# Kernel tuning notes

Measured on AMD Instinct MI355X. Metric: run time of the kernel, lower is better.

Reference implementation:

```python
import jax, jax.numpy as jnp
import numpy as np

N = 4096     # nagents
OBS = 256    # obs_size
HID = 256    # hid_size
G = 64       # gat_hid_size
H1 = 4       # gat_num_heads (so H1*G == HID)
H2 = 1       # gat_num_heads_out
A = 64       # actions
QMAX = 255.0  # 2**quant_bits - 1, quant_min = 0
NEG_SLOPE = 0.2


def _lstm_cell(x, h, c, Wih, Whh, bih, bhh):
    gates = x @ Wih.T + bih + h @ Whh.T + bhh
    i, f, g, o = jnp.split(gates, 4, axis=-1)
    c2 = jax.nn.sigmoid(f) * c + jax.nn.sigmoid(i) * jnp.tanh(g)
    h2 = jax.nn.sigmoid(o) * jnp.tanh(c2)
    return h2, c2


def _gat(x, adj, W, a_i, a_j, b, average, self_loop_type):
    # x: [n, in], adj: [n, n], W: [in, H*g], a_i/a_j: [H, g], b: [H*g] or [g_out]
    n = x.shape[0]
    H, g = a_i.shape
    eye = jnp.eye(n, dtype=adj.dtype)
    if self_loop_type == 1:      # force self-loops
        adj = adj * (1.0 - eye) + eye
    elif self_loop_type == 2:    # remove self-loops
        adj = adj * (1.0 - eye)
    h = (x @ W).reshape(n, H, g)                      # [n, H, g]
    ci = jnp.einsum('nhg,hg->hn', h, a_i)             # [H, n]
    cj = jnp.einsum('nhg,hg->hn', h, a_j)             # [H, n]
    e = jax.nn.leaky_relu(ci[:, :, None] + cj[:, None, :], NEG_SLOPE)  # [H, n, n]
    att = jax.nn.softmax(jnp.where(adj[None] > 0, e, -9e15), axis=-1) * adj[None]
    out = jnp.einsum('hij,jhg->ihg', att, h)          # [n, H, g]
    out = out.mean(axis=1) if average else out.reshape(n, H * g)
    return out + b


def _fake_quant(t, bmask):
    # dynamic-range fake quantization over masked entries (min/max detached)
    big = jnp.asarray(1e30, t.dtype)
    mn = jax.lax.stop_gradient(jnp.min(jnp.where(bmask, t, big)))
    mx = jax.lax.stop_gradient(jnp.max(jnp.where(bmask, t, -big)))
    eq = mn == mx
    mn = jnp.where(eq, mn - 0.01, mn)
    mx = jnp.where(eq, mx + 0.01, mx)
    scale = (mx - mn) / QMAX
    zp = jnp.round(-mn / scale)  # quant_min = 0
    deq = (jnp.clip(jnp.round(t / scale + zp), 0.0, QMAX) - zp) * scale
    return jnp.where(bmask, deq, t)


def _qloss(t, bmask):
    return jnp.sum(jnp.where(bmask, jnp.log2(2.0 * QMAX * jnp.abs(t) + 1.0), 0.0))


def _forward(obs, h0, c0, Wobs, bobs, Wih, Whh, bih, bhh,
             W1, ai1, aj1, b1, W2, ai2, aj2, b2, Wv, bv, Wa, ba):
    n = N
    mask = jnp.ones((n, 1), obs.dtype)        # all agents alive
    enc = obs.reshape(n, -1) @ Wobs + bobs    # obs encoder, squeeze batch=1
    h, c = _lstm_cell(enc, h0, c0, Wih, Whh, bih, bhh)
    comm = h
    bmask = jnp.broadcast_to(mask > 0, comm.shape)
    comm = _fake_quant(comm, bmask)
    loss = _qloss(comm, bmask)
    comm = comm * mask
    adj = jnp.ones((n, n), obs.dtype) * mask * mask.T   # complete graph
    comm = _gat(comm, adj, W1, ai1, aj1, b1, average=False, self_loop_type=1)
    comm = jax.nn.elu(comm)
    bmask2 = jnp.broadcast_to(mask > 0, comm.shape)
    comm = _fake_quant(comm, bmask2)
    loss = loss + _qloss(comm, bmask2)
    comm = _gat(comm, adj, W2, ai2, aj2, b2, average=True, self_loop_type=1)
    comm = comm * mask
    value = jnp.concatenate([h, comm], axis=-1) @ Wv + bv              # [n, 1]
    feat = jnp.concatenate([h.reshape(1, n, -1), comm.reshape(1, n, -1)], axis=-1)
    logp = jax.nn.log_softmax(feat @ Wa + ba, axis=-1)                 # [1, n, A]
    return logp, value, h, c, loss


def setup_inputs() -> dict:
    key = jax.random.key(0)
    ks = jax.random.split(key, 21)
    def rn(k, shape, sc=0.05):
        return jax.random.normal(k, shape, dtype=jnp.float32) * sc
    return {
        'obs': rn(ks[0], (1, N, OBS), 1.0),
        'h0': rn(ks[1], (N, HID), 1.0),
        'c0': rn(ks[2], (N, HID), 1.0),
        'Wobs': rn(ks[3], (OBS, HID)),
        'bobs': rn(ks[4], (HID,)),
        'Wih': rn(ks[5], (4 * HID, HID)),
        'Whh': rn(ks[6], (4 * HID, HID)),
        'bih': rn(ks[7], (4 * HID,)),
        'bhh': rn(ks[8], (4 * HID,)),
        'W1': rn(ks[9], (HID, H1 * G)),
        'ai1': rn(ks[10], (H1, G)),
        'aj1': rn(ks[11], (H1, G)),
        'b1': rn(ks[12], (H1 * G,)),
        'W2': rn(ks[13], (H1 * G, H2 * HID)),
        'ai2': rn(ks[14], (H2, HID)),
        'aj2': rn(ks[15], (H2, HID)),
        'b2': rn(ks[16], (HID,)),
        'Wv': rn(ks[17], (2 * HID, 1)),
        'bv': rn(ks[18], (1,)),
        'Wa': rn(ks[19], (2 * HID, A)),
        'ba': rn(ks[20], (A,)),
    }


def reference(obs, h0, c0, Wobs, bobs, Wih, Whh, bih, bhh,
              W1, ai1, aj1, b1, W2, ai2, aj2, b2, Wv, bv, Wa, ba):
    return _forward(obs, h0, c0, Wobs, bobs, Wih, Whh, bih, bhh,
                    W1, ai1, aj1, b1, W2, ai2, aj2, b2, Wv, bv, Wa, ba)
```

## Files before the change

### kernel.cpp

```cpp
#include <hip/hip_runtime.h>
#include <math.h>

typedef __attribute__((ext_vector_type(8))) short short8;
typedef __attribute__((ext_vector_type(4))) float floatx4;

__device__ __forceinline__ ushort f2b(float f) {
  unsigned u = __float_as_uint(f);
  unsigned r = u + 0x7FFFu + ((u >> 16) & 1u);
  return (ushort)(r >> 16);
}
__device__ __forceinline__ unsigned encf(float f) {
  unsigned u = __float_as_uint(f);
  return (u & 0x80000000u) ? ~u : (u | 0x80000000u);
}
__device__ __forceinline__ float b2f(ushort b) {
  return __uint_as_float(((unsigned)b) << 16);
}

__global__ __launch_bounds__(256) void prep_kernel(
    const float* __restrict__ Wih, ushort* __restrict__ Wihp,
    const float* __restrict__ Whh, ushort* __restrict__ Whhp,
    const float* __restrict__ Wobs, ushort* __restrict__ WobsT,
    const float* __restrict__ W1, ushort* __restrict__ W1T,
    const float* __restrict__ W2, ushort* __restrict__ W2T,
    const float* __restrict__ Wa, const float* __restrict__ Wv,
    const float* __restrict__ ba, const float* __restrict__ bv,
    const float* __restrict__ bih, const float* __restrict__ bhh,
    ushort* __restrict__ WaTe, float* __restrict__ bias_ext, float* __restrict__ bias12,
    const float* __restrict__ ai1, const float* __restrict__ aj1,
    const float* __restrict__ ai2, const float* __restrict__ aj2,
    ushort* __restrict__ wab1, ushort* __restrict__ wab2)
{
  __shared__ float tile[32][33];
  const int bid = blockIdx.x;
  const int tid = threadIdx.x;
  if (bid < 512) {
    const int i = bid * 256 + tid;
    const int half = i >> 16;
    const int ii = i & 65535;
    const int pr = ii >> 6, k4 = ii & 63;
    const int orow = ((pr >> 4) & 3) * 256 + (pr >> 6) * 16 + (pr & 15);
    const float* s = half ? Whh : Wih;
    ushort* d = half ? Whhp : Wihp;
    const float4 v = *(const float4*)(s + (size_t)orow * 256 + k4 * 4);
    ushort4 o; o.x = f2b(v.x); o.y = f2b(v.y); o.z = f2b(v.z); o.w = f2b(v.w);
    *(ushort4*)(d + (size_t)pr * 256 + k4 * 4) = o;
  } else if (bid < 704) {
    const int t = bid - 512;
    const int mat = t >> 6, sub = t & 63;
    const float* in = mat == 0 ? Wobs : (mat == 1 ? W1 : W2);
    ushort* outp = mat == 0 ? WobsT : (mat == 1 ? W1T : W2T);
    const int c0 = (sub & 7) * 32, r0 = (sub >> 3) * 32;
    const int tx = tid & 31, ty = tid >> 5;
    #pragma unroll
    for (int p = 0; p < 32; p += 8)
      tile[ty + p][tx] = in[(size_t)(r0 + ty + p) * 256 + c0 + tx];
    __syncthreads();
    #pragma unroll
    for (int p = 0; p < 32; p += 8)
      outp[(size_t)(c0 + ty + p) * 256 + r0 + tx] = f2b(tile[tx][ty + p]);
  } else if (bid < 965) {
    const int idx = (bid - 704) * 256 + tid;
    if (idx < 65536) {
      const int n = idx >> 9, k = idx & 511;
      const float v = n < 64 ? Wa[(size_t)k * 64 + n] : (n == 64 ? Wv[k] : 0.0f);
      WaTe[idx] = f2b(v);
    } else if (idx < 65536 + 128) {
      const int n = idx - 65536;
      bias_ext[n] = n < 64 ? ba[n] : (n == 64 ? bv[0] : 0.0f);
    } else if (idx < 65536 + 128 + 1024) {
      const int pc = idx - 65536 - 128;
      const int orow = ((pc >> 4) & 3) * 256 + (pc >> 6) * 16 + (pc & 15);
      bias12[pc] = bih[orow] + bhh[orow];
    }
  } else if (bid < 981) {
    const int c = bid - 965;
    const int k = tid;
    float val = 0.0f;
    if (c < 8) {
      const int h = c & 3;
      const float* av = (c < 4) ? ai1 : aj1;
      for (int g = 0; g < 64; ++g)
        val += W1[(size_t)k * 256 + h * 64 + g] * av[h * 64 + g];
    }
    wab1[c * 256 + k] = f2b(val);
  } else {
    const int c = bid - 981;
    const int k = tid;
    float val = 0.0f;
    if (c < 2) {
      const float* av = (c == 0) ? ai2 : aj2;
      for (int g = 0; g < 256; ++g)
        val += W2[(size_t)k * 256 + g] * av[g];
    }
    wab2[c * 256 + k] = f2b(val);
  }
}

__global__ __launch_bounds__(256) void enc_gemm(
    const float* __restrict__ obs, const ushort* __restrict__ WobsT,
    const float* __restrict__ bobs, ushort* __restrict__ enc_bf)
{
  constexpr int LDT = 40;
  __shared__ __align__(16) ushort As[64 * LDT];
  __shared__ __align__(16) ushort Bs[64 * LDT];
  const int tid = threadIdx.x;
  const int wave = tid >> 6, lane = tid & 63;
  const int wr = wave >> 1, wc = wave & 1;
  const int m0 = blockIdx.y * 64, n0 = blockIdx.x * 64;
  floatx4 acc[2][2] = {};
  const int r = tid >> 2, kq = tid & 3;
  const int lm = lane & 15, lq = lane >> 4;
  for (int k0 = 0; k0 < 256; k0 += 32) {
    {
      const float* s = &obs[(size_t)(m0 + r) * 256 + k0 + kq * 8];
      const float4 a = *(const float4*)s;
      const float4 b = *(const float4*)(s + 4);
      ushort4 o1, o2;
      o1.x = f2b(a.x); o1.y = f2b(a.y); o1.z = f2b(a.z); o1.w = f2b(a.w);
      o2.x = f2b(b.x); o2.y = f2b(b.y); o2.z = f2b(b.z); o2.w = f2b(b.w);
      *(ushort4*)&As[r * LDT + kq * 8] = o1;
      *(ushort4*)&As[r * LDT + kq * 8 + 4] = o2;
      *(float4*)&Bs[r * LDT + kq * 8] =
          *(const float4*)&WobsT[(size_t)(n0 + r) * 256 + k0 + kq * 8];
    }
    __syncthreads();
    short8 af[2], bfr[2];
    #pragma unroll
    for (int i = 0; i < 2; ++i)
      af[i] = *(const short8*)&As[(wr * 32 + i * 16 + lm) * LDT + lq * 8];
    #pragma unroll
    for (int j = 0; j < 2; ++j)
      bfr[j] = *(const short8*)&Bs[(wc * 32 + j * 16 + lm) * LDT + lq * 8];
    #pragma unroll
    for (int i = 0; i < 2; ++i)
      #pragma unroll
      for (int j = 0; j < 2; ++j)
        acc[i][j] = __builtin_amdgcn_mfma_f32_16x16x32_bf16(af[i], bfr[j], acc[i][j], 0, 0, 0);
    __syncthreads();
  }
  #pragma unroll
  for (int i = 0; i < 2; ++i)
    #pragma unroll
    for (int j = 0; j < 2; ++j) {
      const int col = n0 + wc * 32 + j * 16 + lm;
      const float badd = bobs[col];
      #pragma unroll
      for (int t = 0; t < 4; ++t) {
        const int row = m0 + wr * 32 + i * 16 + lq * 4 + t;
        enc_bf[(size_t)row * 256 + col] = f2b(acc[i][j][t] + badd);
      }
    }
}

__global__ __launch_bounds__(256) void gates_lstm_kernel(
    const ushort* __restrict__ enc_bf, const ushort* __restrict__ Wihp,
    const float* __restrict__ h0, const ushort* __restrict__ Whhp,
    const float* __restrict__ bias12p, const float* __restrict__ c0,
    float* __restrict__ h_out, float* __restrict__ c_out, ushort* __restrict__ h_bf,
    float* __restrict__ pmn, float* __restrict__ pmx)
{
  constexpr int LDT = 40;
  __shared__ __align__(16) ushort As[128 * LDT];
  __shared__ __align__(16) ushort Bs[128 * LDT];
  __shared__ float smn[4], smx[4];
  const int tid = threadIdx.x;
  const int wave = tid >> 6, lane = tid & 63;
  const int wr = wave >> 1, wc = wave & 1;
  const int m0 = blockIdx.y * 128, n0 = blockIdx.x * 128;
  floatx4 acc[4][4] = {};
  const int r = tid >> 2, kq = tid & 3;
  const int lm = lane & 15, lq = lane >> 4;
  for (int k0 = 0; k0 < 512; k0 += 32) {
    const ushort* B = (k0 < 256) ? Wihp : Whhp;
    const int kk = (k0 < 256) ? k0 : k0 - 256;
    if (k0 < 256) {
      #pragma unroll
      for (int p = 0; p < 2; ++p) {
        const int rr = r + p * 64;
        *(float4*)&As[rr * LDT + kq * 8] =
            *(const float4*)&enc_bf[(size_t)(m0 + rr) * 256 + kk + kq * 8];
      }
    } else {
      #pragma unroll
      for (int p = 0; p < 2; ++p) {
        const int rr = r + p * 64;
        const float* s = &h0[(size_t)(m0 + rr) * 256 + kk + kq * 8];
        const float4 a = *(const float4*)s;
        const float4 b = *(const float4*)(s + 4);
        ushort4 o1, o2;
        o1.x = f2b(a.x); o1.y = f2b(a.y); o1.z = f2b(a.z); o1.w = f2b(a.w);
        o2.x = f2b(b.x); o2.y = f2b(b.y); o2.z = f2b(b.z); o2.w = f2b(b.w);
        *(ushort4*)&As[rr * LDT + kq * 8] = o1;
        *(ushort4*)&As[rr * LDT + kq * 8 + 4] = o2;
      }
    }
    #pragma unroll
    for (int p = 0; p < 2; ++p) {
      const int rr = r + p * 64;
      *(float4*)&Bs[rr * LDT + kq * 8] =
          *(const float4*)&B[(size_t)(n0 + rr) * 256 + kk + kq * 8];
    }
    __syncthreads();
    short8 af[4], bfr[4];
    #pragma unroll
    for (int i = 0; i < 4; ++i)
      af[i] = *(const short8*)&As[(wr * 64 + i * 16 + lm) * LDT + lq * 8];
    #pragma unroll
    for (int j = 0; j < 4; ++j)
      bfr[j] = *(const short8*)&Bs[(wc * 64 + j * 16 + lm) * LDT + lq * 8];
    #pragma unroll
    for (int i = 0; i < 4; ++i)
      #pragma unroll
      for (int j = 0; j < 4; ++j)
        acc[i][j] = __builtin_amdgcn_mfma_f32_16x16x32_bf16(af[i], bfr[j], acc[i][j], 0, 0, 0);
    __syncthreads();
  }
  const int d = (blockIdx.x * 2 + wc) * 16 + lm;
  float b4[4];
  #pragma unroll
  for (int j = 0; j < 4; ++j) b4[j] = bias12p[n0 + wc * 64 + j * 16 + lm];
  float mnl = 3.0e38f, mxl = -3.0e38f;
  #pragma unroll
  for (int i = 0; i < 4; ++i) {
    #pragma unroll
    for (int t = 0; t < 4; ++t) {
      const int row = m0 + wr * 64 + i * 16 + lq * 4 + t;
      const size_t off = (size_t)row * 256 + d;
      const float gi = acc[i][0][t] + b4[0];
      const float gf = acc[i][1][t] + b4[1];
      const float gg = acc[i][2][t] + b4[2];
      const float go = acc[i][3][t] + b4[3];
      const float cc = c0[off];
      const float si = 1.0f / (1.0f + expf(-gi));
      const float sf = 1.0f / (1.0f + expf(-gf));
      const float so = 1.0f / (1.0f + expf(-go));
      const float c2 = sf * cc + si * tanhf(gg);
      const float h2 = so * tanhf(c2);
      h_out[off] = h2;
      c_out[off] = c2;
      h_bf[off] = f2b(h2);
      mnl = fminf(mnl, h2); mxl = fmaxf(mxl, h2);
    }
  }
  #pragma unroll
  for (int o = 32; o > 0; o >>= 1) {
    mnl = fminf(mnl, __shfl_xor(mnl, o));
    mxl = fmaxf(mxl, __shfl_xor(mxl, o));
  }
  if (lane == 0) { smn[wave] = mnl; smx[wave] = mxl; }
  __syncthreads();
  if (tid == 0) {
    const int bid = blockIdx.y * 8 + blockIdx.x;
    pmn[bid] = fminf(fminf(smn[0], smn[1]), fminf(smn[2], smn[3]));
    pmx[bid] = fmaxf(fmaxf(smx[0], smx[1]), fmaxf(smx[2], smx[3]));
  }
}

__global__ __launch_bounds__(256) void quant_kernel(
    const float4* __restrict__ x, ushort* __restrict__ q, int n4,
    const float* __restrict__ pmn, const float* __restrict__ pmx, int np,
    float* __restrict__ part)
{
  __shared__ float smn[4], smx[4], sl[4], bmn, bmx;
  float mn = 3.0e38f, mx = -3.0e38f;
  for (int i = threadIdx.x; i < np; i += 256) {
    mn = fminf(mn, pmn[i]); mx = fmaxf(mx, pmx[i]);
  }
  #pragma unroll
  for (int o = 32; o > 0; o >>= 1) {
    mn = fminf(mn, __shfl_xor(mn, o));
    mx = fmaxf(mx, __shfl_xor(mx, o));
  }
  if ((threadIdx.x & 63) == 0) { smn[threadIdx.x >> 6] = mn; smx[threadIdx.x >> 6] = mx; }
  __syncthreads();
  if (threadIdx.x == 0) {
    bmn = fminf(fminf(smn[0], smn[1]), fminf(smn[2], smn[3]));
    bmx = fmaxf(fmaxf(smx[0], smx[1]), fmaxf(smx[2], smx[3]));
  }
  __syncthreads();
  mn = bmn; mx = bmx;
  if (mn == mx) { mn -= 0.01f; mx += 0.01f; }
  const float scale = (mx - mn) / 255.0f;
  const float zp = rintf(-mn / scale);
  float lsum = 0.0f;
  for (int idx = blockIdx.x * 256 + threadIdx.x; idx < n4; idx += gridDim.x * 256) {
    const float4 t = x[idx];
    float d0, d1, d2, d3;
    { float qq = fminf(fmaxf(rintf(t.x / scale + zp), 0.0f), 255.0f);
      d0 = (qq - zp) * scale; lsum += log2f(510.0f * fabsf(d0) + 1.0f); }
    { float qq = fminf(fmaxf(rintf(t.y / scale + zp), 0.0f), 255.0f);
      d1 = (qq - zp) * scale; lsum += log2f(510.0f * fabsf(d1) + 1.0f); }
    { float qq = fminf(fmaxf(rintf(t.z / scale + zp), 0.0f), 255.0f);
      d2 = (qq - zp) * scale; lsum += log2f(510.0f * fabsf(d2) + 1.0f); }
    { float qq = fminf(fmaxf(rintf(t.w / scale + zp), 0.0f), 255.0f);
      d3 = (qq - zp) * scale; lsum += log2f(510.0f * fabsf(d3) + 1.0f); }
    ushort4 o; o.x = f2b(d0); o.y = f2b(d1); o.z = f2b(d2); o.w = f2b(d3);
    *(ushort4*)(q + (size_t)idx * 4) = o;
  }
  #pragma unroll
  for (int o = 32; o > 0; o >>= 1) lsum += __shfl_xor(lsum, o);
  if ((threadIdx.x & 63) == 0) sl[threadIdx.x >> 6] = lsum;
  __syncthreads();
  if (threadIdx.x == 0) part[blockIdx.x] = sl[0] + sl[1] + sl[2] + sl[3];
}

template<int HN>
__global__ __launch_bounds__(256) void gat_feat_kernel(
    const ushort* __restrict__ Aq, const ushort* __restrict__ WT,
    const ushort* __restrict__ wab,
    float* __restrict__ hout, float* __restrict__ ci, float* __restrict__ cj)
{
  constexpr int LDT = 40;
  __shared__ __align__(16) ushort As[64 * LDT];
  __shared__ __align__(16) ushort Bs[64 * LDT];
  const int bid = blockIdx.x;
  const int tid = threadIdx.x;
  const int wave = tid >> 6, lane = tid & 63;
  const int lm = lane & 15, lq = lane >> 4;
  const int r = tid >> 2, kq = tid & 3;
  if (bid < 256) {
    const int bx = bid & 3, by = bid >> 2;
    const int m0 = by * 64, n0 = bx * 64;
    const int wr = wave >> 1, wc = wave & 1;
    floatx4 acc[2][2] = {};
    for (int k0 = 0; k0 < 256; k0 += 32) {
      *(float4*)&As[r * LDT + kq * 8] =
          *(const float4*)&Aq[(size_t)(m0 + r) * 256 + k0 + kq * 8];
      *(float4*)&Bs[r * LDT + kq * 8] =
          *(const float4*)&WT[(size_t)(n0 + r) * 256 + k0 + kq * 8];
      __syncthreads();
      short8 af[2], bfr[2];
      #pragma unroll
      for (int i = 0; i < 2; ++i)
        af[i] = *(const short8*)&As[(wr * 32 + i * 16 + lm) * LDT + lq * 8];
      #pragma unroll
      for (int j = 0; j < 2; ++j)
        bfr[j] = *(const short8*)&Bs[(wc * 32 + j * 16 + lm) * LDT + lq * 8];
      #pragma unroll
      for (int i = 0; i < 2; ++i)
        #pragma unroll
        for (int j = 0; j < 2; ++j)
          acc[i][j] = __builtin_amdgcn_mfma_f32_16x16x32_bf16(af[i], bfr[j], acc[i][j], 0, 0, 0);
      __syncthreads();
    }
    #pragma unroll
    for (int i = 0; i < 2; ++i)
      #pragma unroll
      for (int j = 0; j < 2; ++j) {
        const int col = n0 + wc * 32 + j * 16 + lm;
        #pragma unroll
        for (int t = 0; t < 4; ++t) {
          const int row = m0 + wr * 32 + i * 16 + lq * 4 + t;
          hout[(size_t)row * 256 + col] = acc[i][j][t];
        }
      }
  } else {
    const int m0 = (bid - 256) * 64;
    floatx4 acc = {0.f, 0.f, 0.f, 0.f};
    for (int k0 = 0; k0 < 256; k0 += 32) {
      *(float4*)&As[r * LDT + kq * 8] =
          *(const float4*)&Aq[(size_t)(m0 + r) * 256 + k0 + kq * 8];
      if (r < 16)
        *(float4*)&Bs[r * LDT + kq * 8] =
            *(const float4*)&wab[(size_t)r * 256 + k0 + kq * 8];
      __syncthreads();
      const short8 af = *(const short8*)&As[(wave * 16 + lm) * LDT + lq * 8];
      const short8 bf = *(const short8*)&Bs[lm * LDT + lq * 8];
      acc = __builtin_amdgcn_mfma_f32_16x16x32_bf16(af, bf, acc, 0, 0, 0);
      __syncthreads();
    }
    #pragma unroll
    for (int t = 0; t < 4; ++t) {
      const int row = m0 + wave * 16 + lq * 4 + t;
      if (lm < HN) ci[lm * 4096 + row] = acc[t];
      else if (lm < 2 * HN) cj[(lm - HN) * 4096 + row] = acc[t];
    }
  }
}

__global__ __launch_bounds__(1024) void rank_sort_kernel(
    const float* __restrict__ c, unsigned* __restrict__ skey,
    float* __restrict__ sc, int* __restrict__ pm)
{
  __shared__ unsigned lk[4096];
  __shared__ int scnt[16][64];
  const int head = blockIdx.x >> 6;
  const int seg = blockIdx.x & 63;
  const float* ch = c + head * 4096;
  for (int idx = threadIdx.x; idx < 4096; idx += 1024)
    lk[idx] = (encf(ch[idx]) & 0xFFFFF000u) | (unsigned)idx;
  __syncthreads();
  const int jl = threadIdx.x & 63;
  const int kg = threadIdx.x >> 6;
  const unsigned my = lk[seg * 64 + jl];
  int cnt = 0;
  const int k0 = kg * 256;
  #pragma unroll 8
  for (int k = k0; k < k0 + 256; ++k)
    cnt += lk[k] < my ? 1 : 0;
  scnt[kg][jl] = cnt;
  __syncthreads();
  if (threadIdx.x < 64) {
    int rank = 0;
    #pragma unroll
    for (int g = 0; g < 16; ++g) rank += scnt[g][threadIdx.x];
    const unsigned kk = lk[seg * 64 + threadIdx.x];
    const int jj = (int)(kk & 0xFFFu);
    skey[head * 4096 + rank] = kk;
    sc[head * 4096 + rank] = ch[jj];
    pm[head * 4096 + rank] = jj;
  }
}

__global__ __launch_bounds__(128) void local_scan1(
    const float* __restrict__ h1, const float* __restrict__ sc, const int* __restrict__ pm,
    float* __restrict__ PUl, float* __restrict__ PVl,
    float* __restrict__ dUl, float* __restrict__ dVl,
    float* __restrict__ cku, float* __restrict__ ckv,
    float* __restrict__ ckus, float* __restrict__ ckvs)
{
  const int head = blockIdx.x >> 6;
  const int chunk = blockIdx.x & 63;
  const int wave = threadIdx.x >> 6;
  const int lane = threadIdx.x & 63;
  const float cmax = sc[head * 4096 + 4095];
  const int base = head * 4096 + chunk * 64;
  const float cv = sc[base + lane];
  const float u = expf(cv - cmax);
  const float v = expf(0.2f * (cv - cmax));
  const int myj = pm[base + lane];
  const float* hrow = h1 + head * 64 + lane;
  if (wave == 0) {
    float iu = u, iv = v;
    #pragma unroll
    for (int o = 1; o < 64; o <<= 1) {
      const float tu = __shfl_up(iu, o), tv = __shfl_up(iv, o);
      if (lane >= o) { iu += tu; iv += tv; }
    }
    const float totU = __shfl(iu, 63), totV = __shfl(iv, 63);
    dVl[base + lane] = iv - v;
    dUl[base + lane] = totU - (iu - u);
    if (lane == 0) { ckus[head * 64 + chunk] = totU; ckvs[head * 64 + chunk] = totV; }
    float accV = 0.f;
    #pragma unroll 16
    for (int k = 0; k < 64; ++k) {
      const float vk = __shfl(v, k);
      const int j = __shfl(myj, k);
      PVl[(size_t)(base + k) * 64 + lane] = accV;
      accV += vk * hrow[(size_t)j * 256];
    }
    ckv[(head * 64 + chunk) * 64 + lane] = accV;
  } else {
    float accU = 0.f;
    #pragma unroll 16
    for (int k = 63; k >= 0; --k) {
      const float uk = __shfl(u, k);
      const int j = __shfl(myj, k);
      accU += uk * hrow[(size_t)j * 256];
      PUl[(size_t)(base + k) * 64 + lane] = accU;
    }
    cku[(head * 64 + chunk) * 64 + lane] = accU;
  }
}

__global__ __launch_bounds__(256) void local_scan2(
    const float* __restrict__ h2, const float* __restrict__ sc, const int* __restrict__ pm,
    float* __restrict__ PUl, float* __restrict__ PVl,
    float* __restrict__ dUl, float* __restrict__ dVl,
    float* __restrict__ cku, float* __restrict__ ckv,
    float* __restrict__ ckus, float* __restrict__ ckvs)
{
  __shared__ float su[64], sv[64];
  __shared__ int sj[64];
  const int chunk = blockIdx.y;
  const int colgrp = blockIdx.x;
  const int tid = threadIdx.x;
  const int wave = tid >> 6, lane = tid & 63;
  const float cmax = sc[4095];
  const int base = chunk * 64;
  if (tid < 64) {
    const float cv = sc[base + tid];
    const float u = expf(cv - cmax);
    const float v = expf(0.2f * (cv - cmax));
    su[tid] = u; sv[tid] = v; sj[tid] = pm[base + tid];
    if (colgrp == 0) {
      float iu = u, iv = v;
      #pragma unroll
      for (int o = 1; o < 64; o <<= 1) {
        const float tu = __shfl_up(iu, o), tv = __shfl_up(iv, o);
        if (lane >= o) { iu += tu; iv += tv; }
      }
      const float totU = __shfl(iu, 63), totV = __shfl(iv, 63);
      dVl[base + lane] = iv - v;
      dUl[base + lane] = totU - (iu - u);
      if (lane == 0) { ckus[chunk] = totU; ckvs[chunk] = totV; }
    }
  }
  __syncthreads();
  const int col = colgrp * 128 + (wave & 1) * 64 + lane;
  if (wave < 2) {
    float accV = 0.f;
    #pragma unroll 16
    for (int k = 0; k < 64; ++k) {
      PVl[(size_t)(base + k) * 256 + col] = accV;
      accV += sv[k] * h2[(size_t)sj[k] * 256 + col];
    }
    ckv[chunk * 256 + col] = accV;
  } else {
    float accU = 0.f;
    #pragma unroll 16
    for (int k = 63; k >= 0; --k) {
      accU += su[k] * h2[(size_t)sj[k] * 256 + col];
      PUl[(size_t)(base + k) * 256 + col] = accU;
    }
    cku[chunk * 256 + col] = accU;
  }
}

__global__ __launch_bounds__(64) void prefix1_kernel(
    const float* __restrict__ cku, const float* __restrict__ ckv,
    const float* __restrict__ ckus, const float* __restrict__ ckvs,
    float* __restrict__ sufU, float* __restrict__ prefV,
    float* __restrict__ sufUs, float* __restrict__ prefVs)
{
  const int head = blockIdx.x, lane = threadIdx.x;
  float acc = 0.f;
  for (int c = 0; c < 64; ++c) {
    prefV[(head * 65 + c) * 64 + lane] = acc;
    acc += ckv[(head * 64 + c) * 64 + lane];
  }
  prefV[(head * 65 + 64) * 64 + lane] = acc;
  acc = 0.f;
  sufU[(head * 65 + 64) * 64 + lane] = 0.f;
  for (int c = 63; c >= 0; --c) {
    acc += cku[(head * 64 + c) * 64 + lane];
    sufU[(head * 65 + c) * 64 + lane] = acc;
  }
  {
    const float vs = ckvs[head * 64 + lane];
    const float us = ckus[head * 64 + lane];
    float iv = vs, iu = us;
    #pragma unroll
    for (int o = 1; o < 64; o <<= 1) {
      const float tv = __shfl_up(iv, o), tu = __shfl_up(iu, o);
      if (lane >= o) { iv += tv; iu += tu; }
    }
    prefVs[head * 65 + lane] = iv - vs;
    const float totU = __shfl(iu, 63);
    sufUs[head * 65 + lane] = totU - iu + us;
    if (lane == 63) {
      prefVs[head * 65 + 64] = iv;
      sufUs[head * 65 + 64] = 0.f;
    }
  }
}

__global__ __launch_bounds__(256) void prefix2_kernel(
    const float* __restrict__ cku, const float* __restrict__ ckv,
    const float* __restrict__ ckus, const float* __restrict__ ckvs,
    float* __restrict__ sufU, float* __restrict__ prefV,
    float* __restrict__ sufUs, float* __restrict__ prefVs)
{
  const int col = threadIdx.x;
  const int lane = col & 63;
  float acc = 0.f;
  for (int c = 0; c < 64; ++c) {
    prefV[c * 256 + col] = acc;
    acc += ckv[c * 256 + col];
  }
  prefV[64 * 256 + col] = acc;
  acc = 0.f;
  sufU[64 * 256 + col] = 0.f;
  for (int c = 63; c >= 0; --c) {
    acc += cku[c * 256 + col];
    sufU[c * 256 + col] = acc;
  }
  if (col < 64) {
    const float vs = ckvs[lane];
    const float us = ckus[lane];
    float iv = vs, iu = us;
    #pragma unroll
    for (int o = 1; o < 64; o <<= 1) {
      const float tv = __shfl_up(iv, o), tu = __shfl_up(iu, o);
      if (lane >= o) { iv += tv; iu += tu; }
    }
    prefVs[lane] = iv - vs;
    const float totU = __shfl(iu, 63);
    sufUs[lane] = totU - iu + us;
    if (lane == 63) { prefVs[64] = iv; sufUs[64] = 0.f; }
  }
}

__global__ __launch_bounds__(256) void combine1_kernel(
    const float* __restrict__ ci, const unsigned* __restrict__ skey,
    const float* __restrict__ sc,
    const float* __restrict__ sufU, const float* __restrict__ prefV,
    const float* __restrict__ sufUs, const float* __restrict__ prefVs,
    const float* __restrict__ PUl, const float* __restrict__ PVl,
    const float* __restrict__ dUl, const float* __restrict__ dVl,
    const float* __restrict__ b1, float* __restrict__ out,
    float* __restrict__ pmn, float* __restrict__ pmx)
{
  const int i = blockIdx.x;
  const int head = threadIdx.x >> 6;
  const int lane = threadIdx.x & 63;
  const unsigned* skh = skey + head * 4096;
  const float civ = ci[head * 4096 + i];
  const float cmax = sc[head * 4096 + 4095];
  const float sarg = civ + cmax;
  const float m = sarg > 0.f ? sarg : 0.2f * sarg;
  const float Af = expf(sarg - m);
  const float Bf = expf(0.2f * sarg - m);
  const unsigned tkey = (encf(-civ) & 0xFFFFF000u) | 0xFFFu;
  int lo = 0, hi = 4096;
  while (lo < hi) {
    const int mid = (lo + hi) >> 1;
    if (skh[mid] > tkey) hi = mid; else lo = mid + 1;
  }
  const int s = lo;
  float accP, accN, dP, dN;
  if (s == 4096) {
    accP = 0.f; dP = 0.f;
    accN = prefV[(head * 65 + 64) * 64 + lane];
    dN = prefVs[head * 65 + 64];
  } else {
    const int cs = s >> 6;
    accP = sufU[(head * 65 + cs + 1) * 64 + lane] + PUl[(size_t)(head * 4096 + s) * 64 + lane];
    accN = prefV[(head * 65 + cs) * 64 + lane] + PVl[(size_t)(head * 4096 + s) * 64 + lane];
    dP = sufUs[head * 65 + cs + 1] + dUl[head * 4096 + s];
    dN = prefVs[head * 65 + cs] + dVl[head * 4096 + s];
  }
  const float num = Af * accP + Bf * accN;
  const float den = Af * dP + Bf * dN;
  const float o = num / den + b1[head * 64 + lane];
  const float oe = o > 0.f ? o : expm1f(o);
  out[(size_t)i * 256 + head * 64 + lane] = oe;
  float mn = oe, mx = oe;
  #pragma unroll
  for (int of = 32; of > 0; of >>= 1) {
    mn = fminf(mn, __shfl_xor(mn, of));
    mx = fmaxf(mx, __shfl_xor(mx, of));
  }
  __shared__ float smn[4], smx[4];
  if (lane == 0) { smn[head] = mn; smx[head] = mx; }
  __syncthreads();
  if (threadIdx.x == 0) {
    pmn[i] = fminf(fminf(smn[0], smn[1]), fminf(smn[2], smn[3]));
    pmx[i] = fmaxf(fmaxf(smx[0], smx[1]), fmaxf(smx[2], smx[3]));
  }
}

__global__ __launch_bounds__(256) void combine2_kernel(
    const float* __restrict__ ci, const unsigned* __restrict__ skey,
    const float* __restrict__ sc,
    const float* __restrict__ sufU, const float* __restrict__ prefV,
    const float* __restrict__ sufUs, const float* __restrict__ prefVs,
    const float* __restrict__ PUl, const float* __restrict__ PVl,
    const float* __restrict__ dUl, const float* __restrict__ dVl,
    const float* __restrict__ b2, ushort* __restrict__ outb)
{
  const int i = blockIdx.x;
  const int col = threadIdx.x;
  const float civ = ci[i];
  const float cmax = sc[4095];
  const float sarg = civ + cmax;
  const float m = sarg > 0.f ? sarg : 0.2f * sarg;
  const float Af = expf(sarg - m);
  const float Bf = expf(0.2f * sarg - m);
  const unsigned tkey = (encf(-civ) & 0xFFFFF000u) | 0xFFFu;
  int lo = 0, hi = 4096;
  while (lo < hi) {
    const int mid = (lo + hi) >> 1;
    if (skey[mid] > tkey) hi = mid; else lo = mid + 1;
  }
  const int s = lo;
  float accP, accN, dP, dN;
  if (s == 4096) {
    accP = 0.f; dP = 0.f;
    accN = prefV[64 * 256 + col];
    dN = prefVs[64];
  } else {
    const int cs = s >> 6;
    accP = sufU[(cs + 1) * 256 + col] + PUl[(size_t)s * 256 + col];
    accN = prefV[cs * 256 + col] + PVl[(size_t)s * 256 + col];
    dP = sufUs[cs + 1] + dUl[s];
    dN = prefVs[cs] + dVl[s];
  }
  const float num = Af * accP + Bf * accN;
  const float den = Af * dP + Bf * dN;
  outb[(size_t)i * 256 + col] = f2b(num / den + b2[col]);
}

__global__ __launch_bounds__(256) void heads_kernel(
    const ushort* __restrict__ h_bf, const ushort* __restrict__ comm2_bf,
    const ushort* __restrict__ WaTe, const float* __restrict__ bias_ext,
    float* __restrict__ out_logp, float* __restrict__ out_value,
    const float* __restrict__ p1, const float* __restrict__ p2,
    float* __restrict__ out_loss)
{
  constexpr int LDT = 40;
  __shared__ __align__(16) ushort As[64 * LDT];
  __shared__ __align__(16) ushort Bs[128 * LDT];
  __shared__ float lbuf[64][68];
  const int tid = threadIdx.x;
  const int wave = tid >> 6, lane = tid & 63;
  const int wr = wave >> 1, wc = wave & 1;
  const int m0 = blockIdx.x * 64;
  const int lm = lane & 15, lq = lane >> 4;
  floatx4 acc[2][4] = {};
  const int r = tid >> 2, kq = tid & 3;
  for (int k0 = 0; k0 < 512; k0 += 32) {
    const ushort* Asrc = (k0 < 256) ? h_bf : comm2_bf;
    const int kk = (k0 < 256) ? k0 : k0 - 256;
    *(float4*)&As[r * LDT + kq * 8] =
        *(const float4*)&Asrc[(size_t)(m0 + r) * 256 + kk + kq * 8];
    #pragma unroll
    for (int p = 0; p < 2; ++p) {
      const int rr = r + p * 64;
      *(float4*)&Bs[rr * LDT + kq * 8] =
          *(const float4*)&WaTe[(size_t)rr * 512 + k0 + kq * 8];
    }
    __syncthreads();
    short8 af[2], bfr[4];
    #pragma unroll
    for (int i = 0; i < 2; ++i)
      af[i] = *(const short8*)&As[(wr * 32 + i * 16 + lm) * LDT + lq * 8];
    #pragma unroll
    for (int j = 0; j < 4; ++j)
      bfr[j] = *(const short8*)&Bs[(wc * 64 + j * 16 + lm) * LDT + lq * 8];
    #pragma unroll
    for (int i = 0; i < 2; ++i)
      #pragma unroll
      for (int j = 0; j < 4; ++j)
        acc[i][j] = __builtin_amdgcn_mfma_f32_16x16x32_bf16(af[i], bfr[j], acc[i][j], 0, 0, 0);
    __syncthreads();
  }
  #pragma unroll
  for (int i = 0; i < 2; ++i)
    #pragma unroll
    for (int j = 0; j < 4; ++j) {
      const int col = wc * 64 + j * 16 + lm;
      if (col < 65) {
        const float badd = bias_ext[col];
        #pragma unroll
        for (int t = 0; t < 4; ++t)
          lbuf[wr * 32 + i * 16 + lq * 4 + t][col] = acc[i][j][t] + badd;
      }
    }
  __syncthreads();
  for (int rr2 = 0; rr2 < 16; ++rr2) {
    const int row = wave * 16 + rr2;
    const float x = lbuf[row][lane];
    float mx = x;
    #pragma unroll
    for (int o = 32; o > 0; o >>= 1) mx = fmaxf(mx, __shfl_xor(mx, o));
    float e = expf(x - mx);
    #pragma unroll
    for (int o = 32; o > 0; o >>= 1) e += __shfl_xor(e, o);
    out_logp[(size_t)(m0 + row) * 64 + lane] = x - mx - logf(e);
    if (lane == 0) out_value[m0 + row] = lbuf[row][64];
  }
  if (blockIdx.x == 0 && wave == 0) {
    float s = 0.f;
    #pragma unroll
    for (int k = 0; k < 4; ++k) s += p1[lane + k * 64] + p2[lane + k * 64];
    #pragma unroll
    for (int o = 32; o > 0; o >>= 1) s += __shfl_xor(s, o);
    if (lane == 0) out_loss[0] = s;
  }
}

extern "C" void kernel_launch(void* const* d_in, const int* in_sizes, int n_in,
                              void* d_out, int out_size, void* d_ws, size_t ws_size,
                              hipStream_t stream) {
  const float* obs  = (const float*)d_in[0];
  const float* h0   = (const float*)d_in[1];
  const float* c0   = (const float*)d_in[2];
  const float* Wobs = (const float*)d_in[3];
  const float* bobs = (const float*)d_in[4];
  const float* Wih  = (const float*)d_in[5];
  const float* Whh  = (const float*)d_in[6];
  const float* bih  = (const float*)d_in[7];
  const float* bhh  = (const float*)d_in[8];
  const float* W1   = (const float*)d_in[9];
  const float* ai1  = (const float*)d_in[10];
  const float* aj1  = (const float*)d_in[11];
  const float* b1   = (const float*)d_in[12];
  const float* W2   = (const float*)d_in[13];
  const float* ai2  = (const float*)d_in[14];
  const float* aj2  = (const float*)d_in[15];
  const float* b2   = (const float*)d_in[16];
  const float* Wv   = (const float*)d_in[17];
  const float* bv   = (const float*)d_in[18];
  const float* Wa   = (const float*)d_in[19];
  const float* ba   = (const float*)d_in[20];

  float* out       = (float*)d_out;
  float* out_logp  = out;
  float* out_value = out + 262144;
  float* out_h     = out + 266240;
  float* out_c     = out + 1314816;
  float* out_loss  = out + 2363392;

  char* ws = (char*)d_ws;
  float* part1  = (float*)(ws + 256);
  float* part2  = (float*)(ws + 1280);
  float* pmn    = (float*)(ws + 2304);
  float* pmx    = (float*)(ws + 18688);
  const size_t MB = 1048576;
  const size_t base = 35072;
  ushort* Wihp    = (ushort*)(ws + base);
  ushort* Whhp    = (ushort*)(ws + base + 524288);
  ushort* WobsT   = (ushort*)(ws + base + 1 * MB);
  ushort* W1T     = (ushort*)(ws + base + 1 * MB + 131072);
  ushort* W2T     = (ushort*)(ws + base + 1 * MB + 262144);
  ushort* WaTe    = (ushort*)(ws + base + 1 * MB + 393216);
  float*  bias_ext= (float*) (ws + base + 1 * MB + 524288);
  float*  bias12  = (float*) (ws + base + 1 * MB + 525312);
  ushort* wab1    = (ushort*)(ws + base + 1 * MB + 532480);
  ushort* wab2    = (ushort*)(ws + base + 1 * MB + 540672);
  ushort* enc_bf  = (ushort*)(ws + base + 2 * MB);
  ushort* h_bf    = (ushort*)(ws + base + 4 * MB);
  ushort* comm_q1 = (ushort*)(ws + base + 6 * MB);
  ushort* comm_q2 = (ushort*)(ws + base + 8 * MB);
  ushort* comm2_bf= (ushort*)(ws + base + 10 * MB);
  float*  h1      = (float*) (ws + base + 12 * MB);
  float*  comm1e  = (float*) (ws + base + 16 * MB);
  float*  h2b     = (float*) (ws + base + 20 * MB);
  size_t so = base + 24 * MB;
  auto alloc = [&](size_t bytes) { size_t r = so; so += (bytes + 255) & ~255ull; return (char*)ws + r; };
  float* ci1    = (float*)alloc(4 * 4096 * 4);
  float* cj1    = (float*)alloc(4 * 4096 * 4);
  unsigned* skey1 = (unsigned*)alloc(4 * 4096 * 4);
  float* sc1    = (float*)alloc(4 * 4096 * 4);
  int*   pm1    = (int*)  alloc(4 * 4096 * 4);
  float* cku1   = (float*)alloc(4 * 64 * 64 * 4);
  float* ckv1   = (float*)alloc(4 * 64 * 64 * 4);
  float* ckus1  = (float*)alloc(4 * 64 * 4);
  float* ckvs1  = (float*)alloc(4 * 64 * 4);
  float* sufU1  = (float*)alloc(4 * 65 * 64 * 4);
  float* prefV1 = (float*)alloc(4 * 65 * 64 * 4);
  float* sufUs1 = (float*)alloc(4 * 65 * 4);
  float* prefVs1= (float*)alloc(4 * 65 * 4);
  float* ci2    = (float*)alloc(4096 * 4);
  float* cj2    = (float*)alloc(4096 * 4);
  unsigned* skey2 = (unsigned*)alloc(4096 * 4);
  float* sc2    = (float*)alloc(4096 * 4);
  int*   pm2    = (int*)  alloc(4096 * 4);
  float* cku2   = (float*)alloc(64 * 256 * 4);
  float* ckv2   = (float*)alloc(64 * 256 * 4);
  float* ckus2  = (float*)alloc(64 * 4);
  float* ckvs2  = (float*)alloc(64 * 4);
  float* sufU2  = (float*)alloc(65 * 256 * 4);
  float* prefV2 = (float*)alloc(65 * 256 * 4);
  float* sufUs2 = (float*)alloc(65 * 4);
  float* prefVs2= (float*)alloc(65 * 4);
  float* PUl    = (float*)alloc(4 * 4096 * 64 * 4);
  float* PVl    = (float*)alloc(4 * 4096 * 64 * 4);
  float* dUl    = (float*)alloc(4 * 4096 * 4);
  float* dVl    = (float*)alloc(4 * 4096 * 4);

  const dim3 b256(256);
  const int N4 = 262144;

  prep_kernel<<<dim3(997), b256, 0, stream>>>(
      Wih, Wihp, Whh, Whhp, Wobs, WobsT, W1, W1T, W2, W2T,
      Wa, Wv, ba, bv, bih, bhh, WaTe, bias_ext, bias12,
      ai1, aj1, ai2, aj2, wab1, wab2);
  enc_gemm<<<dim3(4, 64), b256, 0, stream>>>(obs, WobsT, bobs, enc_bf);
  gates_lstm_kernel<<<dim3(8, 32), b256, 0, stream>>>(
      enc_bf, Wihp, h0, Whhp, bias12, c0, out_h, out_c, h_bf, pmn, pmx);
  quant_kernel<<<dim3(256), b256, 0, stream>>>(
      (const float4*)out_h, comm_q1, N4, pmn, pmx, 256, part1);
  gat_feat_kernel<4><<<dim3(320), b256, 0, stream>>>(
      comm_q1, W1T, wab1, h1, ci1, cj1);
  rank_sort_kernel<<<dim3(256), dim3(1024), 0, stream>>>(cj1, skey1, sc1, pm1);
  local_scan1<<<dim3(256), dim3(128), 0, stream>>>(h1, sc1, pm1,
      PUl, PVl, dUl, dVl, cku1, ckv1, ckus1, ckvs1);
  prefix1_kernel<<<dim3(4), dim3(64), 0, stream>>>(cku1, ckv1, ckus1, ckvs1,
                                                   sufU1, prefV1, sufUs1, prefVs1);
  combine1_kernel<<<dim3(4096), b256, 0, stream>>>(ci1, skey1, sc1,
      sufU1, prefV1, sufUs1, prefVs1, PUl, PVl, dUl, dVl, b1, comm1e, pmn, pmx);
  quant_kernel<<<dim3(256), b256, 0, stream>>>(
      (const float4*)comm1e, comm_q2, N4, pmn, pmx, 4096, part2);
  gat_feat_kernel<1><<<dim3(320), b256, 0, stream>>>(
      comm_q2, W2T, wab2, h2b, ci2, cj2);
  rank_sort_kernel<<<dim3(64), dim3(1024), 0, stream>>>(cj2, skey2, sc2, pm2);
  local_scan2<<<dim3(2, 64), b256, 0, stream>>>(h2b, sc2, pm2,
      PUl, PVl, dUl, dVl, cku2, ckv2, ckus2, ckvs2);
  prefix2_kernel<<<dim3(1), b256, 0, stream>>>(cku2, ckv2, ckus2, ckvs2,
                                               sufU2, prefV2, sufUs2, prefVs2);
  combine2_kernel<<<dim3(4096), b256, 0, stream>>>(ci2, skey2, sc2,
      sufU2, prefV2, sufUs2, prefVs2, PUl, PVl, dUl, dVl, b2, comm2_bf);
  heads_kernel<<<dim3(64), b256, 0, stream>>>(
      h_bf, comm2_bf, WaTe, bias_ext, out_logp, out_value, part1, part2, out_loss);
}
```

Before: 248.0 us.

## Fuse fake-quantization into GAT feature GEMM, vectorize rank sort, retile heads

Drops the two standalone quant kernels. The GAT feature GEMM now reduces the global min/max itself, quantizes the fp32 activations while loading its tiles, and writes per-row-block log-loss partials (only bx==0 blocks contribute, so each element is counted once). This removes two launches and a bf16 round trip through memory. The cost is that each element is quantized four times across the column blocks, plus a redundant min/max reduction in every block. The rank sort also reads keys as uint4 from LDS, and the heads kernel moves to 32-row tiles across 128 blocks with a simpler loss sum over 64 partials.

New measurement: 250.0 us. No clear change (+0.8%).

```diff
diff --git a/kernel.cpp b/kernel.cpp
--- a/kernel.cpp
+++ b/kernel.cpp
@@ -12,9 +12,6 @@
 __device__ __forceinline__ unsigned encf(float f) {
   unsigned u = __float_as_uint(f);
   return (u & 0x80000000u) ? ~u : (u | 0x80000000u);
-}
-__device__ __forceinline__ float b2f(ushort b) {
-  return __uint_as_float(((unsigned)b) << 16);
 }
 
 __global__ __launch_bounds__(256) void prep_kernel(
@@ -257,76 +254,65 @@
   }
 }
 
-__global__ __launch_bounds__(256) void quant_kernel(
-    const float4* __restrict__ x, ushort* __restrict__ q, int n4,
-    const float* __restrict__ pmn, const float* __restrict__ pmx, int np,
-    float* __restrict__ part)
-{
-  __shared__ float smn[4], smx[4], sl[4], bmn, bmx;
-  float mn = 3.0e38f, mx = -3.0e38f;
-  for (int i = threadIdx.x; i < np; i += 256) {
-    mn = fminf(mn, pmn[i]); mx = fmaxf(mx, pmx[i]);
-  }
-  #pragma unroll
-  for (int o = 32; o > 0; o >>= 1) {
-    mn = fminf(mn, __shfl_xor(mn, o));
-    mx = fmaxf(mx, __shfl_xor(mx, o));
-  }
-  if ((threadIdx.x & 63) == 0) { smn[threadIdx.x >> 6] = mn; smx[threadIdx.x >> 6] = mx; }
-  __syncthreads();
-  if (threadIdx.x == 0) {
-    bmn = fminf(fminf(smn[0], smn[1]), fminf(smn[2], smn[3]));
-    bmx = fmaxf(fmaxf(smx[0], smx[1]), fmaxf(smx[2], smx[3]));
-  }
-  __syncthreads();
-  mn = bmn; mx = bmx;
-  if (mn == mx) { mn -= 0.01f; mx += 0.01f; }
-  const float scale = (mx - mn) / 255.0f;
-  const float zp = rintf(-mn / scale);
-  float lsum = 0.0f;
-  for (int idx = blockIdx.x * 256 + threadIdx.x; idx < n4; idx += gridDim.x * 256) {
-    const float4 t = x[idx];
-    float d0, d1, d2, d3;
-    { float qq = fminf(fmaxf(rintf(t.x / scale + zp), 0.0f), 255.0f);
-      d0 = (qq - zp) * scale; lsum += log2f(510.0f * fabsf(d0) + 1.0f); }
-    { float qq = fminf(fmaxf(rintf(t.y / scale + zp), 0.0f), 255.0f);
-      d1 = (qq - zp) * scale; lsum += log2f(510.0f * fabsf(d1) + 1.0f); }
-    { float qq = fminf(fmaxf(rintf(t.z / scale + zp), 0.0f), 255.0f);
-      d2 = (qq - zp) * scale; lsum += log2f(510.0f * fabsf(d2) + 1.0f); }
-    { float qq = fminf(fmaxf(rintf(t.w / scale + zp), 0.0f), 255.0f);
-      d3 = (qq - zp) * scale; lsum += log2f(510.0f * fabsf(d3) + 1.0f); }
-    ushort4 o; o.x = f2b(d0); o.y = f2b(d1); o.z = f2b(d2); o.w = f2b(d3);
-    *(ushort4*)(q + (size_t)idx * 4) = o;
-  }
-  #pragma unroll
-  for (int o = 32; o > 0; o >>= 1) lsum += __shfl_xor(lsum, o);
-  if ((threadIdx.x & 63) == 0) sl[threadIdx.x >> 6] = lsum;
-  __syncthreads();
-  if (threadIdx.x == 0) part[blockIdx.x] = sl[0] + sl[1] + sl[2] + sl[3];
-}
-
 template<int HN>
 __global__ __launch_bounds__(256) void gat_feat_kernel(
-    const ushort* __restrict__ Aq, const ushort* __restrict__ WT,
+    const float* __restrict__ Af32, const ushort* __restrict__ WT,
     const ushort* __restrict__ wab,
+    const float* __restrict__ pmn, const float* __restrict__ pmx, int np,
+    float* __restrict__ part,
     float* __restrict__ hout, float* __restrict__ ci, float* __restrict__ cj)
 {
   constexpr int LDT = 40;
   __shared__ __align__(16) ushort As[64 * LDT];
   __shared__ __align__(16) ushort Bs[64 * LDT];
+  __shared__ float sred[8], s_sz[2];
   const int bid = blockIdx.x;
   const int tid = threadIdx.x;
   const int wave = tid >> 6, lane = tid & 63;
   const int lm = lane & 15, lq = lane >> 4;
   const int r = tid >> 2, kq = tid & 3;
+  {
+    float mn = 3.0e38f, mx = -3.0e38f;
+    for (int i = tid; i < np; i += 256) { mn = fminf(mn, pmn[i]); mx = fmaxf(mx, pmx[i]); }
+    #pragma unroll
+    for (int o = 32; o > 0; o >>= 1) {
+      mn = fminf(mn, __shfl_xor(mn, o)); mx = fmaxf(mx, __shfl_xor(mx, o));
+    }
+    if (lane == 0) { sred[wave] = mn; sred[4 + wave] = mx; }
+    __syncthreads();
+    if (tid == 0) {
+      float bmn = fminf(fminf(sred[0], sred[1]), fminf(sred[2], sred[3]));
+      float bmx = fmaxf(fmaxf(sred[4], sred[5]), fmaxf(sred[6], sred[7]));
+      if (bmn == bmx) { bmn -= 0.01f; bmx += 0.01f; }
+      const float sc = (bmx - bmn) / 255.0f;
+      s_sz[0] = sc; s_sz[1] = rintf(-bmn / sc);
+    }
+    __syncthreads();
+  }
+  const float scale = s_sz[0], zp = s_sz[1];
+  float lsum = 0.0f;
+  auto qz = [&](float t) -> ushort {
+    const float qq = fminf(fmaxf(rintf(t / scale + zp), 0.0f), 255.0f);
+    const float dq = (qq - zp) * scale;
+    lsum += log2f(510.0f * fabsf(dq) + 1.0f);
+    return f2b(dq);
+  };
   if (bid < 256) {
     const int bx = bid & 3, by = bid >> 2;
     const int m0 = by * 64, n0 = bx * 64;
     const int wr = wave >> 1, wc = wave & 1;
     floatx4 acc[2][2] = {};
     for (int k0 = 0; k0 < 256; k0 += 32) {
-      *(float4*)&As[r * LDT + kq * 8] =
-          *(const float4*)&Aq[(size_t)(m0 + r) * 256 + k0 + kq * 8];
+      {
+        const float* s = &Af32[(size_t)(m0 + r) * 256 + k0 + kq * 8];
+        const float4 a = *(const float4*)s;
+        const float4 b = *(const float4*)(s + 4);
+        ushort4 o1, o2;
+        o1.x = qz(a.x); o1.y = qz(a.y); o1.z = qz(a.z); o1.w = qz(a.w);
+        o2.x = qz(b.x); o2.y = qz(b.y); o2.z = qz(b.z); o2.w = qz(b.w);
+        *(ushort4*)&As[r * LDT + kq * 8] = o1;
+        *(ushort4*)&As[r * LDT + kq * 8 + 4] = o2;
+      }
       *(float4*)&Bs[r * LDT + kq * 8] =
           *(const float4*)&WT[(size_t)(n0 + r) * 256 + k0 + kq * 8];
       __syncthreads();
@@ -355,12 +341,28 @@
           hout[(size_t)row * 256 + col] = acc[i][j][t];
         }
       }
+    if (bx == 0) {
+      #pragma unroll
+      for (int o = 32; o > 0; o >>= 1) lsum += __shfl_xor(lsum, o);
+      __syncthreads();
+      if (lane == 0) sred[wave] = lsum;
+      __syncthreads();
+      if (tid == 0) part[by] = sred[0] + sred[1] + sred[2] + sred[3];
+    }
   } else {
     const int m0 = (bid - 256) * 64;
     floatx4 acc = {0.f, 0.f, 0.f, 0.f};
     for (int k0 = 0; k0 < 256; k0 += 32) {
-      *(float4*)&As[r * LDT + kq * 8] =
-          *(const float4*)&Aq[(size_t)(m0 + r) * 256 + k0 + kq * 8];
+      {
+        const float* s = &Af32[(size_t)(m0 + r) * 256 + k0 + kq * 8];
+        const float4 a = *(const float4*)s;
+        const float4 b = *(const float4*)(s + 4);
+        ushort4 o1, o2;
+        o1.x = qz(a.x); o1.y = qz(a.y); o1.z = qz(a.z); o1.w = qz(a.w);
+        o2.x = qz(b.x); o2.y = qz(b.y); o2.z = qz(b.z); o2.w = qz(b.w);
+        *(ushort4*)&As[r * LDT + kq * 8] = o1;
+        *(ushort4*)&As[r * LDT + kq * 8 + 4] = o2;
+      }
       if (r < 16)
         *(float4*)&Bs[r * LDT + kq * 8] =
             *(const float4*)&wab[(size_t)r * 256 + k0 + kq * 8];
@@ -383,7 +385,7 @@
     const float* __restrict__ c, unsigned* __restrict__ skey,
     float* __restrict__ sc, int* __restrict__ pm)
 {
-  __shared__ unsigned lk[4096];
+  __shared__ __align__(16) unsigned lk[4096];
   __shared__ int scnt[16][64];
   const int head = blockIdx.x >> 6;
   const int seg = blockIdx.x & 63;
@@ -395,10 +397,14 @@
   const int kg = threadIdx.x >> 6;
   const unsigned my = lk[seg * 64 + jl];
   int cnt = 0;
-  const int k0 = kg * 256;
+  const uint4* lk4 = (const uint4*)lk;
+  const int k40 = kg * 64;
   #pragma unroll 8
-  for (int k = k0; k < k0 + 256; ++k)
-    cnt += lk[k] < my ? 1 : 0;
+  for (int k4 = k40; k4 < k40 + 64; ++k4) {
+    const uint4 kv = lk4[k4];
+    cnt += (kv.x < my ? 1 : 0) + (kv.y < my ? 1 : 0)
+         + (kv.z < my ? 1 : 0) + (kv.w < my ? 1 : 0);
+  }
   scnt[kg][jl] = cnt;
   __syncthreads();
   if (threadIdx.x < 64) {
@@ -700,21 +706,22 @@
     float* __restrict__ out_loss)
 {
   constexpr int LDT = 40;
-  __shared__ __align__(16) ushort As[64 * LDT];
+  __shared__ __align__(16) ushort As[32 * LDT];
   __shared__ __align__(16) ushort Bs[128 * LDT];
-  __shared__ float lbuf[64][68];
+  __shared__ float lbuf[32][68];
   const int tid = threadIdx.x;
   const int wave = tid >> 6, lane = tid & 63;
   const int wr = wave >> 1, wc = wave & 1;
-  const int m0 = blockIdx.x * 64;
+  const int m0 = blockIdx.x * 32;
   const int lm = lane & 15, lq = lane >> 4;
-  floatx4 acc[2][4] = {};
+  floatx4 acc[4] = {};
   const int r = tid >> 2, kq = tid & 3;
   for (int k0 = 0; k0 < 512; k0 += 32) {
     const ushort* Asrc = (k0 < 256) ? h_bf : comm2_bf;
     const int kk = (k0 < 256) ? k0 : k0 - 256;
-    *(float4*)&As[r * LDT + kq * 8] =
-        *(const float4*)&Asrc[(size_t)(m0 + r) * 256 + kk + kq * 8];
+    if (tid < 128)
+      *(float4*)&As[r * LDT + kq * 8] =
+          *(const float4*)&Asrc[(size_t)(m0 + r) * 256 + kk + kq * 8];
     #pragma unroll
     for (int p = 0; p < 2; ++p) {
       const int rr = r + p * 64;
@@ -722,35 +729,29 @@
           *(const float4*)&WaTe[(size_t)rr * 512 + k0 + kq * 8];
     }
     __syncthreads();
-    short8 af[2], bfr[4];
-    #pragma unroll
-    for (int i = 0; i < 2; ++i)
-      af[i] = *(const short8*)&As[(wr * 32 + i * 16 + lm) * LDT + lq * 8];
+    const short8 af = *(const short8*)&As[(wr * 16 + lm) * LDT + lq * 8];
+    short8 bfr[4];
     #pragma unroll
     for (int j = 0; j < 4; ++j)
       bfr[j] = *(const short8*)&Bs[(wc * 64 + j * 16 + lm) * LDT + lq * 8];
     #pragma unroll
-    for (int i = 0; i < 2; ++i)
-      #pragma unroll
-      for (int j = 0; j < 4; ++j)
-        acc[i][j] = __builtin_amdgcn_mfma_f32_16x16x32_bf16(af[i], bfr[j], acc[i][j], 0, 0, 0);
+    for (int j = 0; j < 4; ++j)
+      acc[j] = __builtin_amdgcn_mfma_f32_16x16x32_bf16(af, bfr[j], acc[j], 0, 0, 0);
     __syncthreads();
   }
   #pragma unroll
-  for (int i = 0; i < 2; ++i)
-    #pragma unroll
-    for (int j = 0; j < 4; ++j) {
-      const int col = wc * 64 + j * 16 + lm;
-      if (col < 65) {
-        const float badd = bias_ext[col];
-        #pragma unroll
-        for (int t = 0; t < 4; ++t)
-          lbuf[wr * 32 + i * 16 + lq * 4 + t][col] = acc[i][j][t] + badd;
-      }
-    }
+  for (int j = 0; j < 4; ++j) {
+    const int col = wc * 64 + j * 16 + lm;
+    if (col < 65) {
+      const float badd = bias_ext[col];
+      #pragma unroll
+      for (int t = 0; t < 4; ++t)
+        lbuf[wr * 16 + lq * 4 + t][col] = acc[j][t] + badd;
+    }
+  }
   __syncthreads();
-  for (int rr2 = 0; rr2 < 16; ++rr2) {
-    const int row = wave * 16 + rr2;
+  for (int rr2 = 0; rr2 < 8; ++rr2) {
+    const int row = wave * 8 + rr2;
     const float x = lbuf[row][lane];
     float mx = x;
     #pragma unroll
@@ -762,9 +763,7 @@
     if (lane == 0) out_value[m0 + row] = lbuf[row][64];
   }
   if (blockIdx.x == 0 && wave == 0) {
-    float s = 0.f;
-    #pragma unroll
-    for (int k = 0; k < 4; ++k) s += p1[lane + k * 64] + p2[lane + k * 64];
+    float s = p1[lane] + p2[lane];
     #pragma unroll
     for (int o = 32; o > 0; o >>= 1) s += __shfl_xor(s, o);
     if (lane == 0) out_loss[0] = s;
@@ -822,13 +821,11 @@
   ushort* wab2    = (ushort*)(ws + base + 1 * MB + 540672);
   ushort* enc_bf  = (ushort*)(ws + base + 2 * MB);
   ushort* h_bf    = (ushort*)(ws + base + 4 * MB);
-  ushort* comm_q1 = (ushort*)(ws + base + 6 * MB);
-  ushort* comm_q2 = (ushort*)(ws + base + 8 * MB);
-  ushort* comm2_bf= (ushort*)(ws + base + 10 * MB);
-  float*  h1      = (float*) (ws + base + 12 * MB);
-  float*  comm1e  = (float*) (ws + base + 16 * MB);
-  float*  h2b     = (float*) (ws + base + 20 * MB);
-  size_t so = base + 24 * MB;
+  ushort* comm2_bf= (ushort*)(ws + base + 6 * MB);
+  float*  h1      = (float*) (ws + base + 8 * MB);
+  float*  comm1e  = (float*) (ws + base + 12 * MB);
+  float*  h2b     = (float*) (ws + base + 16 * MB);
+  size_t so = base + 20 * MB;
   auto alloc = [&](size_t bytes) { size_t r = so; so += (bytes + 255) & ~255ull; return (char*)ws + r; };
   float* ci1    = (float*)alloc(4 * 4096 * 4);
   float* cj1    = (float*)alloc(4 * 4096 * 4);
@@ -862,7 +859,6 @@
   float* dVl    = (float*)alloc(4 * 4096 * 4);
 
   const dim3 b256(256);
-  const int N4 = 262144;
 
   prep_kernel<<<dim3(997), b256, 0, stream>>>(
       Wih, Wihp, Whh, Whhp, Wobs, WobsT, W1, W1T, W2, W2T,
@@ -871,10 +867,8 @@
   enc_gemm<<<dim3(4, 64), b256, 0, stream>>>(obs, WobsT, bobs, enc_bf);
   gates_lstm_kernel<<<dim3(8, 32), b256, 0, stream>>>(
       enc_bf, Wihp, h0, Whhp, bias12, c0, out_h, out_c, h_bf, pmn, pmx);
-  quant_kernel<<<dim3(256), b256, 0, stream>>>(
-      (const float4*)out_h, comm_q1, N4, pmn, pmx, 256, part1);
   gat_feat_kernel<4><<<dim3(320), b256, 0, stream>>>(
-      comm_q1, W1T, wab1, h1, ci1, cj1);
+      out_h, W1T, wab1, pmn, pmx, 256, part1, h1, ci1, cj1);
   rank_sort_kernel<<<dim3(256), dim3(1024), 0, stream>>>(cj1, skey1, sc1, pm1);
   local_scan1<<<dim3(256), dim3(128), 0, stream>>>(h1, sc1, pm1,
       PUl, PVl, dUl, dVl, cku1, ckv1, ckus1, ckvs1);
@@ -882,10 +876,8 @@
                                                    sufU1, prefV1, sufUs1, prefVs1);
   combine1_kernel<<<dim3(4096), b256, 0, stream>>>(ci1, skey1, sc1,
       sufU1, prefV1, sufUs1, prefVs1, PUl, PVl, dUl, dVl, b1, comm1e, pmn, pmx);
-  quant_kernel<<<dim3(256), b256, 0, stream>>>(
-      (const float4*)comm1e, comm_q2, N4, pmn, pmx, 4096, part2);
   gat_feat_kernel<1><<<dim3(320), b256, 0, stream>>>(
-      comm_q2, W2T, wab2, h2b, ci2, cj2);
+      comm1e, W2T, wab2, pmn, pmx, 4096, part2, h2b, ci2, cj2);
   rank_sort_kernel<<<dim3(64), dim3(1024), 0, stream>>>(cj2, skey2, sc2, pm2);
   local_scan2<<<dim3(2, 64), b256, 0, stream>>>(h2b, sc2, pm2,
       PUl, PVl, dUl, dVl, cku2, ckv2, ckus2, ckvs2);
@@ -893,6 +885,6 @@
                                                sufU2, prefV2, sufUs2, prefVs2);
   combine2_kernel<<<dim3(4096), b256, 0, stream>>>(ci2, skey2, sc2,
       sufU2, prefV2, sufUs2, prefVs2, PUl, PVl, dUl, dVl, b2, comm2_bf);
-  heads_kernel<<<dim3(64), b256, 0, stream>>>(
+  heads_kernel<<<dim3(128), b256, 0, stream>>>(
       h_bf, comm2_bf, WaTe, bias_ext, out_logp, out_value, part1, part2, out_loss);
 }
```
